# Kernel tuning notes

Measured on AMD Instinct MI355X. Metric: run time of the kernel, lower is better.

The kernel has to match this reference:

```python
import jax, jax.numpy as jnp
import numpy as np

EPS = 1e-12
N, C, B = 8, 2048, 2048


def setup_inputs() -> dict:
    key = jax.random.key(0)
    kx, kk, kq = jax.random.split(key, 3)
    # Xavier-uniform bound for [C,C] weight
    bound = float(np.sqrt(6.0 / (C + C)))
    X = jax.random.normal(kx, (N, C, B), dtype=jnp.float32)
    Wk = jax.random.uniform(kk, (C, C), minval=-bound, maxval=bound, dtype=jnp.float32)
    Wq = jax.random.uniform(kq, (C, C), minval=-bound, maxval=bound, dtype=jnp.float32)
    Wk0 = jnp.zeros((C, 1), dtype=jnp.float32)
    Wq0 = jnp.zeros((C, 1), dtype=jnp.float32)
    return {"X": X, "Wk": Wk, "Wq": Wq, "Wk0": Wk0, "Wq0": Wq0}


def reference(X, Wk, Wq, Wk0, Wq0):
    # X: [N,C,B]; Wk,Wq: [C,C]; Wk0,Wq0: [C,1] (broadcast over B)
    K = jnp.einsum('ij,njb->nib', Wk, X) + Wk0  # [N,C,B]
    Q = jnp.einsum('ij,njb->nib', Wq, X) + Wq0  # [N,C,B]
    DK2 = jnp.sum(K * K, axis=2)  # [N,C] squared row norms
    DQ2 = jnp.sum(Q * Q, axis=2)  # [N,C]
    DQK = jnp.sqrt(jnp.maximum(DQ2[:, :, None] * DK2[:, None, :], EPS))  # [N,C,C]
    Y = jnp.einsum('nib,njb->nij', Q, K) / DQK  # cosine-normalized scores [N,C,C]
    SM = jax.nn.softmax(Y, axis=1)  # softmax over query-channel axis
    # Z = (X^T @ SM)^T : Z[n,j,b] = sum_c X[n,c,b] * SM[n,c,j]
    Z = jnp.einsum('ncb,ncj->njb', X, SM)  # [N,C,B]
    return Z
```

## Files before the change

### kernel.cpp

```cpp
#include <hip/hip_runtime.h>
#include <hip/hip_bf16.h>

typedef __bf16 bf16_t;
typedef __bf16 bf16x8 __attribute__((ext_vector_type(8)));
typedef __bf16 bf16x4 __attribute__((ext_vector_type(4)));
typedef float  f32x4  __attribute__((ext_vector_type(4)));

#define NB 8
#define CD 2048
#define BD 2048
#define LD 2048
#define BK 64
#define NT (LD / BK)
#define NP (NT / 2)

#define BAR()     __builtin_amdgcn_s_barrier()
#define WAITV(n)  asm volatile("s_waitcnt vmcnt(" #n ")" ::: "memory")

__global__ void k_transpose_x(const float* __restrict__ X, bf16_t* __restrict__ XbT) {
    __shared__ bf16_t tile[64][66];
    const int t = threadIdx.x;
    const int b0 = blockIdx.x * 64, c0 = blockIdx.y * 64, n = blockIdx.z;
    const float* Xn = X + (size_t)n * CD * BD;
    bf16_t* Tn = XbT + (size_t)n * BD * CD;
    const int cl = t & 63, rw = t >> 6;
#pragma unroll
    for (int r = 0; r < 16; ++r) {
        int row = r * 4 + rw;
        tile[row][cl] = (bf16_t)Xn[(size_t)(c0 + row) * BD + b0 + cl];
    }
    __syncthreads();
#pragma unroll
    for (int r = 0; r < 16; ++r) {
        int row = r * 4 + rw;
        Tn[(size_t)(b0 + row) * CD + c0 + cl] = tile[cl][row];
    }
}

__global__ void k_convert_w(const float* __restrict__ Wk, const float* __restrict__ Wq,
                            bf16_t* __restrict__ Wkb, bf16_t* __restrict__ Wqb) {
    const size_t i = ((size_t)blockIdx.x * 256 + threadIdx.x) * 4;
    const float* src = blockIdx.y ? Wq : Wk;
    bf16_t* dst = blockIdx.y ? Wqb : Wkb;
    float4 v = *(const float4*)(src + i);
    bf16x4 o;
    o[0] = (bf16_t)v.x; o[1] = (bf16_t)v.y; o[2] = (bf16_t)v.z; o[3] = (bf16_t)v.w;
    *(bf16x4*)(dst + i) = o;
}


__device__ __forceinline__ void gll16(const bf16_t* g, bf16_t* l) {
    __builtin_amdgcn_global_load_lds((const __attribute__((address_space(1))) void*)g,
                                     (__attribute__((address_space(3))) void*)l, 16, 0, 0);
}

__device__ __forceinline__ void stage_half(const bf16_t* gsrc, bf16_t* ldsh, int w, int l) {
    const int rr = l >> 3;
    const int ce = ((l & 7) ^ rr) * 8;
#pragma unroll
    for (int i = 0; i < 2; ++i) {
        const bf16_t* g = gsrc + (size_t)(i * 64 + w * 8 + rr) * LD + ce;
        gll16(g, ldsh + i * 4096 + w * 512);
    }
}

__device__ __forceinline__ bf16x8 lds_frag(const bf16_t* hbase, int row16, int lr, int st, int ks, int swz) {
    const int r = row16 + lr;
    const int ce = (st * 32 + ks * 8) ^ swz;
    return *(const bf16x8*)(hbase + r * 64 + ce);
}

template <int EPI>
__global__ __launch_bounds__(512, 2) void k_gemm256(const bf16_t* __restrict__ Aall, size_t sA,
                                                    const bf16_t* __restrict__ Ball, size_t sB,
                                                    void* __restrict__ Call, size_t sC,
                                                    const float* __restrict__ bias) {
    __shared__ alignas(16) bf16_t As[2][2][128 * 64];
    __shared__ alignas(16) bf16_t Bs[2][2][128 * 64];
    const int tid = threadIdx.x;
    const int lane = tid & 63, wave = tid >> 6;
    const int wm = wave >> 2, wn = wave & 3;
    const int lr = lane & 15, ks = lane >> 4;
    const int swz = (lr & 7) << 3;

    const int bid = blockIdx.x;
    const int lin = (bid & 7) * 64 + (bid >> 3);
    const int z = lin >> 6, rem = lin & 63, bm = rem >> 3, bn = rem & 7;
    const int m0 = bm * 256, n0 = bn * 256;

    const bf16_t* Ab = Aall + sA * z + (size_t)m0 * LD;
    const bf16_t* Bb = Ball + sB * z + (size_t)n0 * LD;

    stage_half(Ab,                 &As[0][0][0], wave, lane);
    stage_half(Bb,                 &Bs[0][0][0], wave, lane);
    stage_half(Ab + 128 * LD,      &As[0][1][0], wave, lane);
    stage_half(Bb + 128 * LD,      &Bs[0][1][0], wave, lane);
    WAITV(4);
    stage_half(Ab + BK,            &As[1][0][0], wave, lane);
    stage_half(Bb + BK,            &Bs[1][0][0], wave, lane);
    stage_half(Bb + 128 * LD + BK, &Bs[1][1][0], wave, lane);
    WAITV(6);
    BAR();

    f32x4 acc[2][2][4][2] = {};
    bf16x8 afrE[4][2], afrO[4][2], bf0[2][2], bf1[2][2];

    auto RD_A = [&](bf16x8 (&dst)[4][2], int slot, int half) {
#pragma unroll
        for (int mi = 0; mi < 4; ++mi)
#pragma unroll
            for (int st = 0; st < 2; ++st)
                dst[mi][st] = lds_frag(&As[slot][half][0], wm * 64 + mi * 16, lr, st, ks, swz);
    };
    auto RD_B = [&](bf16x8 (&dst)[2][2], int slot, int half) {
#pragma unroll
        for (int ni = 0; ni < 2; ++ni)
#pragma unroll
            for (int st = 0; st < 2; ++st)
                dst[ni][st] = lds_frag(&Bs[slot][half][0], wn * 32 + ni * 16, lr, st, ks, swz);
    };
    auto MFMA_Q = [&](int mh, int nh, bf16x8 (&asrc)[4][2], bf16x8 (&bsrc)[2][2]) {
        __builtin_amdgcn_s_setprio(1);
#pragma unroll
        for (int st = 0; st < 2; ++st)
#pragma unroll
            for (int mi = 0; mi < 4; ++mi)
#pragma unroll
                for (int ni = 0; ni < 2; ++ni)
                    acc[mh][nh][mi][ni] = __builtin_amdgcn_mfma_f32_16x16x32_bf16(
                        asrc[mi][st], bsrc[ni][st], acc[mh][nh][mi][ni], 0, 0, 0);
        __builtin_amdgcn_s_setprio(0);
    };

    RD_A(afrE, 0, 0); RD_B(bf0, 0, 0);

    for (int tp = 0; tp < NP; ++tp) {
        const int u = 2 * tp, v = u + 1;
        const int w = (u + 2 < NT) ? u + 2 : NT - 1;
        const int x = (v + 2 < NT) ? v + 2 : NT - 1;

        RD_B(bf1, 0, 1);
        stage_half(Ab + 128 * LD + v * BK, &As[1][1][0], wave, lane);
        BAR();
        MFMA_Q(0, 0, afrE, bf0);
        BAR();

        RD_A(afrO, 0, 1);
        stage_half(Ab + w * BK, &As[0][0][0], wave, lane);
        BAR();
        MFMA_Q(0, 1, afrE, bf1);
        BAR();

        stage_half(Bb + w * BK, &Bs[0][0][0], wave, lane);
        BAR();
        MFMA_Q(1, 0, afrO, bf0);
        BAR();

        stage_half(Bb + 128 * LD + w * BK, &Bs[0][1][0], wave, lane);
        WAITV(6);
        BAR();
        RD_A(afrE, 1, 0); RD_B(bf0, 1, 0);
        MFMA_Q(1, 1, afrO, bf1);
        BAR();

        RD_B(bf1, 1, 1);
        stage_half(Ab + 128 * LD + w * BK, &As[0][1][0], wave, lane);
        BAR();
        MFMA_Q(0, 0, afrE, bf0);
        BAR();

        RD_A(afrO, 1, 1);
        stage_half(Ab + x * BK, &As[1][0][0], wave, lane);
        BAR();
        MFMA_Q(0, 1, afrE, bf1);
        BAR();

        stage_half(Bb + x * BK, &Bs[1][0][0], wave, lane);
        BAR();
        MFMA_Q(1, 0, afrO, bf0);
        BAR();

        stage_half(Bb + 128 * LD + x * BK, &Bs[1][1][0], wave, lane);
        WAITV(6);
        BAR();
        RD_A(afrE, 0, 0); RD_B(bf0, 0, 0);
        MFMA_Q(1, 1, afrO, bf1);
        BAR();
    }
    WAITV(0);

    const int rsub = ks * 4;
#pragma unroll
    for (int mh = 0; mh < 2; ++mh)
#pragma unroll
        for (int mi = 0; mi < 4; ++mi)
#pragma unroll
            for (int j = 0; j < 4; ++j) {
                const int r = m0 + mh * 128 + wm * 64 + mi * 16 + rsub + j;
                float bv = 0.f;
                if (EPI == 1) bv = bias[r];
#pragma unroll
                for (int nh = 0; nh < 2; ++nh)
#pragma unroll
                    for (int ni = 0; ni < 2; ++ni) {
                        const int c = n0 + nh * 128 + wn * 32 + ni * 16 + lr;
                        const float vv = acc[mh][nh][mi][ni][j] + bv;
                        if (EPI == 0) ((float*)Call)[sC * z + (size_t)r * LD + c] = vv;
                        else          ((bf16_t*)Call)[sC * z + (size_t)r * LD + c] = (bf16_t)vv;
                    }
            }
}

__global__ void k_row_norm2(const bf16_t* __restrict__ Kb, const bf16_t* __restrict__ Qb,
                            float* __restrict__ DK2, float* __restrict__ DQ2) {
    const int row = blockIdx.x, n = blockIdx.y;
    const bf16_t* src = blockIdx.z ? Qb : Kb;
    float* dst = blockIdx.z ? DQ2 : DK2;
    const bf16_t* pr = src + ((size_t)n * CD + row) * BD + threadIdx.x * 8;
    bf16x8 v = *(const bf16x8*)pr;
    float s = 0.f;
#pragma unroll
    for (int e = 0; e < 8; ++e) { float x = (float)v[e]; s += x * x; }
#pragma unroll
    for (int off = 32; off; off >>= 1) s += __shfl_xor(s, off, 64);
    __shared__ float ws[4];
    if ((threadIdx.x & 63) == 0) ws[threadIdx.x >> 6] = s;
    __syncthreads();
    if (threadIdx.x == 0) dst[(size_t)n * CD + row] = ws[0] + ws[1] + ws[2] + ws[3];
}

__global__ void k_softmax_rows(const bf16_t* __restrict__ Yt, const float* __restrict__ DK2,
                               const float* __restrict__ DQ2, bf16_t* __restrict__ SMT) {
    const int j = blockIdx.x, n = blockIdx.y, t = threadIdx.x;
    const int lane = t & 63, wave = t >> 6;
    const bf16_t* y = Yt + ((size_t)n * CD + j) * CD;
    const float* q2 = DQ2 + (size_t)n * CD;
    const float dk2 = DK2[(size_t)n * CD + j];
    const int i0 = t * 8;

    bf16x8 yr = *(const bf16x8*)(y + i0);
    float4 qa = *(const float4*)(q2 + i0);
    float4 qb = *(const float4*)(q2 + i0 + 4);
    float qv[8] = {qa.x, qa.y, qa.z, qa.w, qb.x, qb.y, qb.z, qb.w};
    float v[8];
#pragma unroll
    for (int e = 0; e < 8; ++e)
        v[e] = (float)yr[e] * rsqrtf(fmaxf(dk2 * qv[e], 1e-12f));

    float m = v[0];
#pragma unroll
    for (int e = 1; e < 8; ++e) m = fmaxf(m, v[e]);
#pragma unroll
    for (int off = 32; off; off >>= 1) m = fmaxf(m, __shfl_xor(m, off, 64));
    __shared__ float redm[4], reds[4];
    if (lane == 0) redm[wave] = m;
    __syncthreads();
    m = fmaxf(fmaxf(redm[0], redm[1]), fmaxf(redm[2], redm[3]));

    float e8[8];
    float s = 0.f;
#pragma unroll
    for (int e = 0; e < 8; ++e) { e8[e] = __expf(v[e] - m); s += e8[e]; }
#pragma unroll
    for (int off = 32; off; off >>= 1) s += __shfl_xor(s, off, 64);
    if (lane == 0) reds[wave] = s;
    __syncthreads();
    s = reds[0] + reds[1] + reds[2] + reds[3];
    const float inv = 1.f / s;

    bf16x8 o;
#pragma unroll
    for (int e = 0; e < 8; ++e) o[e] = (bf16_t)(e8[e] * inv);
    *(bf16x8*)(SMT + ((size_t)n * CD + j) * CD + i0) = o;
}

extern "C" void kernel_launch(void* const* d_in, const int* in_sizes, int n_in,
                              void* d_out, int out_size, void* d_ws, size_t ws_size,
                              hipStream_t stream) {
    const float* X   = (const float*)d_in[0];
    const float* Wk  = (const float*)d_in[1];
    const float* Wq  = (const float*)d_in[2];
    const float* Wk0 = (const float*)d_in[3];
    const float* Wq0 = (const float*)d_in[4];
    float* Z = (float*)d_out;

    const size_t NCB = (size_t)NB * CD * BD;
    const size_t CC  = (size_t)CD * CD;
    const size_t NCC = (size_t)NB * CC;

    char* p = (char*)d_ws;
    bf16_t* XbT = (bf16_t*)p; p += NCB * 2;
    bf16_t* Wkb = (bf16_t*)p; p += CC * 2;
    bf16_t* Wqb = (bf16_t*)p; p += CC * 2;
    bf16_t* Kb  = (bf16_t*)p; p += NCB * 2;
    bf16_t* Qb  = (bf16_t*)p; p += NCB * 2;
    float*  DK2 = (float*)p;  p += (size_t)NB * CD * 4;
    float*  DQ2 = (float*)p;  p += (size_t)NB * CD * 4;
    bf16_t* Yt  = (bf16_t*)p; p += NCC * 2;
    bf16_t* SMT = Kb;
    if ((size_t)(p - (char*)d_ws) > ws_size) return;

    dim3 blk(256);
    k_transpose_x<<<dim3(BD / 64, CD / 64, NB), blk, 0, stream>>>(X, XbT);
    k_convert_w<<<dim3(CC / 1024, 2), blk, 0, stream>>>(Wk, Wq, Wkb, Wqb);
    k_gemm256<1><<<512, 512, 0, stream>>>(Wkb, 0, XbT, (size_t)BD * CD, Kb, (size_t)CD * BD, Wk0);
    k_gemm256<1><<<512, 512, 0, stream>>>(Wqb, 0, XbT, (size_t)BD * CD, Qb, (size_t)CD * BD, Wq0);
    k_row_norm2<<<dim3(CD, NB, 2), blk, 0, stream>>>(Kb, Qb, DK2, DQ2);
    k_gemm256<2><<<512, 512, 0, stream>>>(Kb, (size_t)CD * BD, Qb, (size_t)CD * BD, Yt, CC, nullptr);
    k_softmax_rows<<<dim3(CD, NB), blk, 0, stream>>>(Yt, DK2, DQ2, SMT);
    k_gemm256<0><<<512, 512, 0, stream>>>(SMT, CC, XbT, (size_t)BD * CD, Z, (size_t)CD * BD, nullptr);
}
```

Before: 577.6 us.

## Restructure GEMM main loop into four phases with scheduled LDS-MFMA interleaving

Reorganizes the bf16 GEMM main loop from eight barrier-separated MFMA quadrants into four phases. Each phase issues two global stage loads, waits, then computes two quadrants. Fragment reads for the next phase are interleaved with MFMAs via sched_group_barrier hints. The aim is to halve barrier count and hide LDS read latency behind matrix ops. In exchange it uses extra fragment registers and changes the vmcnt wait accounting, which could hurt occupancy or correctness if the counts are wrong.

```diff
diff --git a/kernel.cpp b/kernel.cpp
--- a/kernel.cpp
+++ b/kernel.cpp
@@ -16,6 +16,16 @@
 
 #define BAR()     __builtin_amdgcn_s_barrier()
 #define WAITV(n)  asm volatile("s_waitcnt vmcnt(" #n ")" ::: "memory")
+#define M_DSRD 0x100
+#define M_MFMA 0x008
+
+__device__ __forceinline__ void ilv_pattern() {
+#pragma unroll
+    for (int g = 0; g < 4; ++g) {
+        __builtin_amdgcn_sched_group_barrier(M_DSRD, 3, 0);
+        __builtin_amdgcn_sched_group_barrier(M_MFMA, 8, 0);
+    }
+}
 
 __global__ void k_transpose_x(const float* __restrict__ X, bf16_t* __restrict__ XbT) {
     __shared__ bf16_t tile[64][66];
@@ -93,17 +103,17 @@
 
     stage_half(Ab,                 &As[0][0][0], wave, lane);
     stage_half(Bb,                 &Bs[0][0][0], wave, lane);
+    stage_half(Bb + 128 * LD,      &Bs[0][1][0], wave, lane);
     stage_half(Ab + 128 * LD,      &As[0][1][0], wave, lane);
-    stage_half(Bb + 128 * LD,      &Bs[0][1][0], wave, lane);
-    WAITV(4);
     stage_half(Ab + BK,            &As[1][0][0], wave, lane);
     stage_half(Bb + BK,            &Bs[1][0][0], wave, lane);
     stage_half(Bb + 128 * LD + BK, &Bs[1][1][0], wave, lane);
-    WAITV(6);
+    stage_half(Ab + 128 * LD + BK, &As[1][1][0], wave, lane);
+    WAITV(8);
     BAR();
 
     f32x4 acc[2][2][4][2] = {};
-    bf16x8 afrE[4][2], afrO[4][2], bf0[2][2], bf1[2][2];
+    bf16x8 afrE[4][2], afrO[4][2], bE0[2][2], bE1[2][2], bO0[2][2], bO1[2][2];
 
     auto RD_A = [&](bf16x8 (&dst)[4][2], int slot, int half) {
 #pragma unroll
@@ -119,72 +129,75 @@
             for (int st = 0; st < 2; ++st)
                 dst[ni][st] = lds_frag(&Bs[slot][half][0], wn * 32 + ni * 16, lr, st, ks, swz);
     };
-    auto MFMA_Q = [&](int mh, int nh, bf16x8 (&asrc)[4][2], bf16x8 (&bsrc)[2][2]) {
+    auto MFMA2 = [&](int mh, bf16x8 (&asrc)[4][2], bf16x8 (&b0src)[2][2], bf16x8 (&b1src)[2][2]) {
+#pragma unroll
+        for (int st = 0; st < 2; ++st)
+#pragma unroll
+            for (int mi = 0; mi < 4; ++mi) {
+#pragma unroll
+                for (int ni = 0; ni < 2; ++ni)
+                    acc[mh][0][mi][ni] = __builtin_amdgcn_mfma_f32_16x16x32_bf16(
+                        asrc[mi][st], b0src[ni][st], acc[mh][0][mi][ni], 0, 0, 0);
+#pragma unroll
+                for (int ni = 0; ni < 2; ++ni)
+                    acc[mh][1][mi][ni] = __builtin_amdgcn_mfma_f32_16x16x32_bf16(
+                        asrc[mi][st], b1src[ni][st], acc[mh][1][mi][ni], 0, 0, 0);
+            }
+    };
+
+    RD_A(afrE, 0, 0); RD_B(bE0, 0, 0); RD_B(bE1, 0, 1);
+
+    for (int tp = 0; tp < NP; ++tp) {
+        const int u = 2 * tp;
+        const int w = (u + 2 < NT) ? u + 2 : NT - 1;
+        const int x = (u + 3 < NT) ? u + 3 : NT - 1;
+
+        stage_half(Ab + w * BK, &As[0][0][0], wave, lane);
+        stage_half(Bb + w * BK, &Bs[0][0][0], wave, lane);
+        WAITV(8);
+        BAR();
         __builtin_amdgcn_s_setprio(1);
-#pragma unroll
-        for (int st = 0; st < 2; ++st)
-#pragma unroll
-            for (int mi = 0; mi < 4; ++mi)
-#pragma unroll
-                for (int ni = 0; ni < 2; ++ni)
-                    acc[mh][nh][mi][ni] = __builtin_amdgcn_mfma_f32_16x16x32_bf16(
-                        asrc[mi][st], bsrc[ni][st], acc[mh][nh][mi][ni], 0, 0, 0);
+        RD_A(afrO, 0, 1);
+        RD_B(bO0, 1, 0);
+        MFMA2(0, afrE, bE0, bE1);
+        ilv_pattern();
         __builtin_amdgcn_s_setprio(0);
-    };
-
-    RD_A(afrE, 0, 0); RD_B(bf0, 0, 0);
-
-    for (int tp = 0; tp < NP; ++tp) {
-        const int u = 2 * tp, v = u + 1;
-        const int w = (u + 2 < NT) ? u + 2 : NT - 1;
-        const int x = (v + 2 < NT) ? v + 2 : NT - 1;
-
-        RD_B(bf1, 0, 1);
-        stage_half(Ab + 128 * LD + v * BK, &As[1][1][0], wave, lane);
-        BAR();
-        MFMA_Q(0, 0, afrE, bf0);
-        BAR();
-
-        RD_A(afrO, 0, 1);
-        stage_half(Ab + w * BK, &As[0][0][0], wave, lane);
-        BAR();
-        MFMA_Q(0, 1, afrE, bf1);
-        BAR();
-
-        stage_half(Bb + w * BK, &Bs[0][0][0], wave, lane);
-        BAR();
-        MFMA_Q(1, 0, afrO, bf0);
         BAR();
 
         stage_half(Bb + 128 * LD + w * BK, &Bs[0][1][0], wave, lane);
-        WAITV(6);
-        BAR();
-        RD_A(afrE, 1, 0); RD_B(bf0, 1, 0);
-        MFMA_Q(1, 1, afrO, bf1);
-        BAR();
-
-        RD_B(bf1, 1, 1);
         stage_half(Ab + 128 * LD + w * BK, &As[0][1][0], wave, lane);
-        BAR();
-        MFMA_Q(0, 0, afrE, bf0);
-        BAR();
-
+        WAITV(8);
+        BAR();
+        __builtin_amdgcn_s_setprio(1);
+        RD_A(afrE, 1, 0);
+        RD_B(bO1, 1, 1);
+        MFMA2(1, afrO, bE0, bE1);
+        ilv_pattern();
+        __builtin_amdgcn_s_setprio(0);
+        BAR();
+
+        stage_half(Ab + x * BK, &As[1][0][0], wave, lane);
+        stage_half(Bb + x * BK, &Bs[1][0][0], wave, lane);
+        WAITV(8);
+        BAR();
+        __builtin_amdgcn_s_setprio(1);
         RD_A(afrO, 1, 1);
-        stage_half(Ab + x * BK, &As[1][0][0], wave, lane);
-        BAR();
-        MFMA_Q(0, 1, afrE, bf1);
-        BAR();
-
-        stage_half(Bb + x * BK, &Bs[1][0][0], wave, lane);
-        BAR();
-        MFMA_Q(1, 0, afrO, bf0);
+        RD_B(bE0, 0, 0);
+        MFMA2(0, afrE, bO0, bO1);
+        ilv_pattern();
+        __builtin_amdgcn_s_setprio(0);
         BAR();
 
         stage_half(Bb + 128 * LD + x * BK, &Bs[1][1][0], wave, lane);
-        WAITV(6);
-        BAR();
-        RD_A(afrE, 0, 0); RD_B(bf0, 0, 0);
-        MFMA_Q(1, 1, afrO, bf1);
+        stage_half(Ab + 128 * LD + x * BK, &As[1][1][0], wave, lane);
+        WAITV(10);
+        BAR();
+        __builtin_amdgcn_s_setprio(1);
+        RD_A(afrE, 0, 0);
+        RD_B(bE1, 0, 1);
+        MFMA2(1, afrO, bO0, bO1);
+        ilv_pattern();
+        __builtin_amdgcn_s_setprio(0);
         BAR();
     }
     WAITV(0);
```

Measured after the change: 617.2 us. +6.8%, slower.
